# Kernel optimization log

Hardware: AMD Instinct MI355X
Metric: run time of the kernel (lower is better)

## Reference

```python
import jax, jax.numpy as jnp
import numpy as np

C, H, K, G = 256, 8, 32, 8
HD = C // H
SCALE = HD ** -0.5
POS_BND = int(0.8 * K * 1 ** 0.5)  # 25
RPE_NUM = 2 * POS_BND + 1          # 51
NW = 4096


def setup_inputs() -> dict:
    key = jax.random.key(0)
    ks = jax.random.split(key, 8)
    data = jax.random.normal(ks[0], (NW * (K + G), C), dtype=jnp.float32)
    # relative xyz offsets between points in a window; exercise the clamp
    rel_pos = jax.random.randint(ks[1], (NW, K, K, 3), -POS_BND - 5, POS_BND + 6).astype(jnp.int32)
    # additive mask: 0 for valid pairs, -100 for masked (padded) pairs
    keep = jax.random.bernoulli(ks[2], 0.9, (NW, K + G, K + G))
    mask = jnp.where(keep, 0.0, -100.0).astype(jnp.float32)
    qkv_w = jax.random.normal(ks[3], (C, 3 * C), dtype=jnp.float32) * (C ** -0.5)
    qkv_b = jnp.zeros((3 * C,), dtype=jnp.float32)
    proj_w = jax.random.normal(ks[4], (C, C), dtype=jnp.float32) * (C ** -0.5)
    proj_b = jnp.zeros((C,), dtype=jnp.float32)
    rpe_table = jax.random.normal(ks[5], (3 * RPE_NUM, H), dtype=jnp.float32) * 0.02
    return {"data": data, "rel_pos": rel_pos, "mask": mask, "qkv_w": qkv_w,
            "qkv_b": qkv_b, "proj_w": proj_w, "proj_b": proj_b, "rpe_table": rpe_table}


def reference(data, rel_pos, mask, qkv_w, qkv_b, proj_w, proj_b, rpe_table):
    W = K + G  # window size including context tokens
    qkv = data @ qkv_w + qkv_b                              # (T, 3C)
    qkv_std = jnp.std(qkv, axis=0, ddof=1)                  # torch .std is unbiased
    qkv = qkv.reshape(-1, W, 3, H, HD).transpose(2, 0, 3, 1, 4)  # (3, Nw, H, W, HD)
    q, k, v = qkv[0] * SCALE, qkv[1], qkv[2]
    attn = jnp.einsum('nhqd,nhkd->nhqk', q, k)              # (Nw, H, W, W)
    # RPE: clamp offsets, index per-axis slices of table, sum over xyz
    idx = jnp.clip(rel_pos, -POS_BND, POS_BND) + POS_BND + jnp.arange(3, dtype=rel_pos.dtype) * RPE_NUM
    rpe = rpe_table[idx].sum(axis=3)                        # (Nw, K, K, H)
    rpe = rpe.transpose(0, 3, 1, 2)                         # (Nw, H, K, K)
    rpe = jnp.pad(rpe, ((0, 0), (0, 0), (G, 0), (G, 0)))    # pad for context tokens
    attn = attn + rpe + mask[:, None]
    attn = jax.nn.softmax(attn, axis=-1)
    out = jnp.einsum('nhqk,nhkd->nqhd', attn, v).reshape(-1, W, C)
    out = out @ proj_w + proj_b                             # (Nw, W, C)
    return (out, qkv_std)
```

## Files before the change

### kernel.cpp

```cpp
#include <hip/hip_runtime.h>
#include <math.h>

#define SCALE_F 0.17677669529663687f

typedef __bf16 bf16x8 __attribute__((ext_vector_type(8)));
typedef float f32x4 __attribute__((ext_vector_type(4)));

__device__ __forceinline__ unsigned short f2bf(float f) {
  unsigned u = __builtin_bit_cast(unsigned, f);
  u = (u + 0x7FFFu + ((u >> 16) & 1u)) >> 16;
  return (unsigned short)u;
}
__device__ __forceinline__ float bf2f(unsigned short u) {
  return __builtin_bit_cast(float, (unsigned)u << 16);
}
__device__ __forceinline__ unsigned pk2(float a, float b) {
  return (unsigned)f2bf(a) | ((unsigned)f2bf(b) << 16);
}
__device__ __forceinline__ bf16x8 ld16(const void* p) {
  int4 v = *(const int4*)p;
  return __builtin_bit_cast(bf16x8, v);
}
__device__ __forceinline__ void gll16(const void* g, void* l) {
  __builtin_amdgcn_global_load_lds(
      (const __attribute__((address_space(1))) unsigned int*)g,
      (__attribute__((address_space(3))) unsigned int*)l, 16, 0, 0);
}


__global__ void octa_prep2(const float* __restrict__ qkv_w, const float* __restrict__ proj_w,
                           unsigned short* __restrict__ wTq, unsigned short* __restrict__ pTq)
{
  int e = blockIdx.x * 256 + threadIdx.x;
  if (e < 196608) {
    int nh = e / 98304, rr = e % 98304;
    int kc = rr / 12288, p2 = rr % 12288;
    int n = p2 >> 5, cw = p2 & 31;
    int kl = cw ^ (((n >> 1) & 3) << 3);
    wTq[e] = f2bf(qkv_w[(size_t)(kc * 32 + kl) * 768 + nh * 384 + n]);
  } else {
    int e2 = e - 196608;
    int kc = e2 >> 13, p2 = e2 & 8191;
    int n = p2 >> 5, cw = p2 & 31;
    int kl = cw ^ (((n >> 1) & 3) << 3);
    pTq[e2] = f2bf(proj_w[(size_t)(kc * 32 + kl) * 256 + n]);
  }
}

#define K1_A0 0
#define K1_A1 4096
#define K1_B0 8192
#define K1_B1 32768
#define K1_LDS 57344

__global__ __launch_bounds__(512, 4)
void octa_qkv(const float* __restrict__ data, const float* __restrict__ qkv_b,
              const unsigned short* __restrict__ wTq, float* __restrict__ ws,
              char* __restrict__ qg, char* __restrict__ kg, char* __restrict__ vg)
{
  extern __shared__ char smem[];
  const int tid = threadIdx.x, lane = tid & 63, wid = tid >> 6;
  const int ql = lane & 15, lg = lane >> 4;
  const int bm = blockIdx.x >> 1, nh = blockIdx.x & 1;
  const int wr = wid >> 2, wc = wid & 3;

  const int arow = tid >> 3, acq = tid & 7;
  const float* abase = data + ((size_t)bm * 64 + arow) * 256 + acq * 4;
  const int alds = arow * 64 + ((acq * 8) ^ (((arow >> 1) & 3) << 4));
  const char* wbase = (const char*)wTq + (size_t)nh * 196608;

  float4 arr0 = *(const float4*)(abase);
  float4 arr1 = *(const float4*)(abase + 32);
  #pragma unroll
  for (int it = 0; it < 3; ++it)
    gll16(wbase + wid * 3072 + it * 1024 + lane * 16,
          smem + K1_B0 + wid * 3072 + it * 1024);
  *(uint2*)(smem + K1_A0 + alds) = make_uint2(pk2(arr0.x, arr0.y), pk2(arr0.z, arr0.w));
  __syncthreads();

  f32x4 acc[2][6];
  #pragma unroll
  for (int m = 0; m < 2; ++m)
    #pragma unroll
    for (int n = 0; n < 6; ++n) acc[m][n] = (f32x4){0.f, 0.f, 0.f, 0.f};

  #pragma unroll
  for (int t = 0; t < 8; ++t) {
    if (t < 6) {
      float4 tmp = *(const float4*)(abase + (t + 2) * 32);
      if ((t & 1) == 0) arr0 = tmp; else arr1 = tmp;
    }
    if (t < 7) {
      char* bb1 = smem + (((t + 1) & 1) ? K1_B1 : K1_B0);
      #pragma unroll
      for (int it = 0; it < 3; ++it)
        gll16(wbase + (size_t)(t + 1) * 24576 + wid * 3072 + it * 1024 + lane * 16,
              bb1 + wid * 3072 + it * 1024);
    }
    const char* ab = smem + ((t & 1) ? K1_A1 : K1_A0);
    const char* bb = smem + ((t & 1) ? K1_B1 : K1_B0);
    bf16x8 af[2];
    #pragma unroll
    for (int mt = 0; mt < 2; ++mt) {
      int row = wr * 32 + mt * 16 + ql;
      af[mt] = ld16(ab + row * 64 + ((lg * 16) ^ (((row >> 1) & 3) << 4)));
    }
    #pragma unroll
    for (int nt = 0; nt < 6; ++nt) {
      int n = wc * 96 + nt * 16 + ql;
      bf16x8 bf = ld16(bb + n * 64 + ((lg * 16) ^ (((n >> 1) & 3) << 4)));
      #pragma unroll
      for (int mt = 0; mt < 2; ++mt)
        acc[mt][nt] = __builtin_amdgcn_mfma_f32_16x16x32_bf16(af[mt], bf, acc[mt][nt], 0, 0, 0);
    }
    if (t < 7) {
      float4 av = ((t + 1) & 1) ? arr1 : arr0;
      *(uint2*)(smem + ((t & 1) ? K1_A0 : K1_A1) + alds) =
          make_uint2(pk2(av.x, av.y), pk2(av.z, av.w));
    }
    __syncthreads();
  }

  #pragma unroll
  for (int nt = 0; nt < 6; ++nt) {
    int colg = nh * 384 + wc * 96 + nt * 16 + ql;
    int tensor = colg >> 8, h = (colg >> 5) & 7, d = colg & 31;
    float bias = qkv_b[colg];
    float s1 = 0.f, s2 = 0.f;
    #pragma unroll
    for (int mt = 0; mt < 2; ++mt) {
      float v4[4];
      #pragma unroll
      for (int r = 0; r < 4; ++r) {
        float v = acc[mt][nt][r] + bias;
        s1 += v; s2 += v * v;
        v4[r] = v;
      }
      int tg0 = bm * 64 + wr * 32 + mt * 16 + lg * 4;
      int w = tg0 / 40, tk0 = tg0 - w * 40;
      size_t slice = (size_t)(w * 8 + h) * 2560;
      if (tensor == 0) {
        #pragma unroll
        for (int r = 0; r < 4; ++r)
          *(unsigned short*)(qg + slice + (tk0 + r) * 64 + d * 2) = f2bf(v4[r] * SCALE_F);
      } else if (tensor == 1) {
        #pragma unroll
        for (int r = 0; r < 4; ++r)
          *(unsigned short*)(kg + slice + (tk0 + r) * 64 + d * 2) = f2bf(v4[r]);
      } else {
        *(uint2*)(vg + slice + d * 80 + tk0 * 2) =
            make_uint2(pk2(v4[0], v4[1]), pk2(v4[2], v4[3]));
      }
    }
    s1 += __shfl_xor(s1, 16); s1 += __shfl_xor(s1, 32);
    s2 += __shfl_xor(s2, 16); s2 += __shfl_xor(s2, 32);
    if (lg == 0) { atomicAdd(ws + colg, s1); atomicAdd(ws + 768 + colg, s2); }
  }
}

#define A2_MSK 0
#define A2_IDX 4160
#define A2_RPT 8256
#define A2_P   13376
#define A2_LDS 44096

__global__ __launch_bounds__(512, 4)
void octa_attn(const char* __restrict__ qg, const char* __restrict__ kg,
               const char* __restrict__ vg, const float* __restrict__ maskp,
               const int* __restrict__ rel_pos, const float* __restrict__ rpe_table,
               char* __restrict__ Og)
{
  extern __shared__ char smem[];
  const int tid = threadIdx.x, w = blockIdx.x, wid = tid >> 6;
  const int lane = tid & 63, ql = lane & 15, lg = lane >> 4, h = wid;
  const int perm = ql * 64 + lg * 16;
  const int vperm = ql * 80 + lg * 16;
  const char* qb = qg + (size_t)(w * 8 + h) * 2560;
  const char* kb = kg + (size_t)(w * 8 + h) * 2560;
  const char* vb = vg + (size_t)(w * 8 + h) * 2560;

  bf16x8 kf0 = ld16(kb + perm), kf1 = ld16(kb + 1024 + perm), kf2 = ld16(kb + 2048 + perm);
  bf16x8 qf0 = ld16(qb + perm), qf1 = ld16(qb + 1024 + perm), qf2 = ld16(qb + 2048 + perm);
  bf16x8 vA = ld16(vb + vperm);
  bf16x8 vB = ld16(vb + 1280 + vperm);
  bf16x8 vC = ld16(vb + 64 + vperm);
  bf16x8 vD = ld16(vb + 1280 + 64 + vperm);
  if (lg != 0) {
    int4 z = {0, 0, 0, 0};
    vC = __builtin_bit_cast(bf16x8, z);
    vD = __builtin_bit_cast(bf16x8, z);
  }

  for (int f = tid; f < 1600; f += 512) {
    float m = maskp[(size_t)w * 1600 + f];
    int qi = f / 40, kj = f - qi * 40;
    *(unsigned short*)(smem + A2_MSK + kj * 104 + qi * 2) = f2bf(m);
  }
  for (int f = tid; f < 1024; f += 512) {
    const int* rp = rel_pos + ((size_t)w * 1024 + f) * 3;
    int c0 = rp[0], c1 = rp[1], c2 = rp[2];
    c0 = min(25, max(-25, c0)); c1 = min(25, max(-25, c1)); c2 = min(25, max(-25, c2));
    unsigned pk = (unsigned)(c0 + 25) | ((unsigned)(c1 + 76) << 10) | ((unsigned)(c2 + 127) << 20);
    int qi8 = f >> 5, kj8 = f & 31;
    *(unsigned*)(smem + A2_IDX + kj8 * 128 + ((qi8 * 4) ^ ((kj8 & 1) << 6))) = pk;
  }
  for (int f = tid; f < 1224; f += 512)
    *(float*)(smem + A2_RPT + (((f & 7) * 160 + (f >> 3)) << 2)) = rpe_table[f];
  __syncthreads();

  f32x4 st[9];
  {
    bf16x8 kf[3] = {kf0, kf1, kf2}, qf[3] = {qf0, qf1, qf2};
    #pragma unroll
    for (int a = 0; a < 3; ++a)
      #pragma unroll
      for (int b = 0; b < 3; ++b)
        st[a * 3 + b] = __builtin_amdgcn_mfma_f32_16x16x32_bf16(
            kf[a], qf[b], (f32x4){0.f, 0.f, 0.f, 0.f}, 0, 0, 0);
  }

  float mx[3] = {-3e38f, -3e38f, -3e38f};
  #pragma unroll
  for (int a = 0; a < 3; ++a) {
    #pragma unroll
    for (int b = 0; b < 3; ++b) {
      #pragma unroll
      for (int r = 0; r < 4; ++r) {
        int kj = a * 16 + lg * 4 + r;
        int qi = b * 16 + ql;
        float s = st[a * 3 + b][r];
        if (kj < 40) {
          if (qi < 40) {
            s += bf2f(*(const unsigned short*)(smem + A2_MSK + kj * 104 + qi * 2));
            if (kj >= 8 && qi >= 8) {
              unsigned pk = *(const unsigned*)(smem + A2_IDX + (kj - 8) * 128 +
                                               (((qi - 8) * 4) ^ (((kj - 8) & 1) << 6)));
              s += *(const float*)(smem + A2_RPT + ((h * 160 + (pk & 1023)) << 2))
                 + *(const float*)(smem + A2_RPT + ((h * 160 + ((pk >> 10) & 1023)) << 2))
                 + *(const float*)(smem + A2_RPT + ((h * 160 + (pk >> 20)) << 2));
            }
          }
        } else {
          s = -1e30f;
        }
        st[a * 3 + b][r] = s;
        mx[b] = fmaxf(mx[b], s);
      }
    }
  }
  #pragma unroll
  for (int b = 0; b < 3; ++b) {
    mx[b] = fmaxf(mx[b], __shfl_xor(mx[b], 16));
    mx[b] = fmaxf(mx[b], __shfl_xor(mx[b], 32));
  }
  float sum[3] = {0.f, 0.f, 0.f};
  #pragma unroll
  for (int a = 0; a < 3; ++a)
    #pragma unroll
    for (int b = 0; b < 3; ++b)
      #pragma unroll
      for (int r = 0; r < 4; ++r) {
        float e = __expf(st[a * 3 + b][r] - mx[b]);
        st[a * 3 + b][r] = e;
        sum[b] += e;
      }
  float inv[3];
  #pragma unroll
  for (int b = 0; b < 3; ++b) {
    sum[b] += __shfl_xor(sum[b], 16);
    sum[b] += __shfl_xor(sum[b], 32);
    inv[b] = 1.f / sum[b];
  }

  char* pb_ = smem + A2_P + wid * 3840;
  f32x4 ot[6];
  #pragma unroll
  for (int i = 0; i < 6; ++i) ot[i] = (f32x4){0.f, 0.f, 0.f, 0.f};

  #pragma unroll
  for (int a = 0; a < 2; ++a)
    #pragma unroll
    for (int b = 0; b < 3; ++b)
      #pragma unroll
      for (int r = 0; r < 4; ++r) {
        int kj = a * 16 + lg * 4 + r, qi = b * 16 + ql;
        *(unsigned short*)(pb_ + qi * 80 + kj * 2) = f2bf(st[a * 3 + b][r] * inv[b]);
      }
  asm volatile("" ::: "memory");
  #pragma unroll
  for (int b = 0; b < 3; ++b) {
    bf16x8 pf = ld16(pb_ + (b * 16 + ql) * 80 + lg * 16);
    ot[b]     = __builtin_amdgcn_mfma_f32_16x16x32_bf16(vA, pf, ot[b], 0, 0, 0);
    ot[3 + b] = __builtin_amdgcn_mfma_f32_16x16x32_bf16(vB, pf, ot[3 + b], 0, 0, 0);
  }
  asm volatile("" ::: "memory");
  #pragma unroll
  for (int b = 0; b < 3; ++b) {
    int qi = b * 16 + ql;
    #pragma unroll
    for (int r = 0; r < 4; ++r)
      *(unsigned short*)(pb_ + qi * 80 + (lg * 4 + r) * 2) = f2bf(st[6 + b][r] * inv[b]);
    *(uint2*)(pb_ + qi * 80 + 32 + lg * 8) = make_uint2(0u, 0u);
  }
  asm volatile("" ::: "memory");
  #pragma unroll
  for (int b = 0; b < 3; ++b) {
    bf16x8 pf = ld16(pb_ + (b * 16 + ql) * 80 + lg * 16);
    ot[b]     = __builtin_amdgcn_mfma_f32_16x16x32_bf16(vC, pf, ot[b], 0, 0, 0);
    ot[3 + b] = __builtin_amdgcn_mfma_f32_16x16x32_bf16(vD, pf, ot[3 + b], 0, 0, 0);
  }

  __syncthreads();
  #pragma unroll
  for (int dm = 0; dm < 2; ++dm)
    #pragma unroll
    for (int b = 0; b < 3; ++b) {
      int qi = b * 16 + ql;
      if (b == 2 && ql >= 8) continue;
      unsigned u0 = pk2(ot[dm * 3 + b][0], ot[dm * 3 + b][1]);
      unsigned u1 = pk2(ot[dm * 3 + b][2], ot[dm * 3 + b][3]);
      int tg = w * 40 + qi;
      int colb = (h * 32 + dm * 16 + lg * 4) * 2;
      *(uint2*)(Og + (size_t)tg * 512 + (colb ^ (((tg >> 1) & 3) << 4))) = make_uint2(u0, u1);
    }
}

#define P3_A0 0
#define P3_A1 8192
#define P3_B0 16384
#define P3_B1 32768
#define P3_LDS 49152

__global__ __launch_bounds__(512, 4)
void octa_proj(const char* __restrict__ Og, const unsigned short* __restrict__ pTq,
               const float* __restrict__ proj_b, float* __restrict__ out)
{
  extern __shared__ char smem[];
  const int tid = threadIdx.x, lane = tid & 63, wid = tid >> 6;
  const int ql = lane & 15, lg = lane >> 4;
  const int bm = blockIdx.x;
  const int wr = wid >> 2, wc = wid & 3;
  const char* pbase = (const char*)pTq;

  gll16(Og + ((size_t)bm * 128 + (tid >> 2)) * 512 + (tid & 3) * 16,
        smem + P3_A0 + wid * 1024);
  #pragma unroll
  for (int it = 0; it < 2; ++it)
    gll16(pbase + (wid * 128 + it * 64 + lane) * 16, smem + P3_B0 + wid * 2048 + it * 1024);
  __syncthreads();

  f32x4 acc[4][4];
  #pragma unroll
  for (int m = 0; m < 4; ++m)
    #pragma unroll
    for (int n = 0; n < 4; ++n) acc[m][n] = (f32x4){0.f, 0.f, 0.f, 0.f};

  #pragma unroll
  for (int t = 0; t < 8; ++t) {
    if (t < 7) {
      char* ab1 = smem + (((t + 1) & 1) ? P3_A1 : P3_A0);
      char* bb1 = smem + (((t + 1) & 1) ? P3_B1 : P3_B0);
      gll16(Og + ((size_t)bm * 128 + (tid >> 2)) * 512 + (t + 1) * 64 + (tid & 3) * 16,
            ab1 + wid * 1024);
      #pragma unroll
      for (int it = 0; it < 2; ++it)
        gll16(pbase + (size_t)(t + 1) * 16384 + (wid * 128 + it * 64 + lane) * 16,
              bb1 + wid * 2048 + it * 1024);
    }
    const char* ab = smem + ((t & 1) ? P3_A1 : P3_A0);
    const char* bb = smem + ((t & 1) ? P3_B1 : P3_B0);
    bf16x8 af[4];
    #pragma unroll
    for (int mt = 0; mt < 4; ++mt) {
      int row = wr * 64 + mt * 16 + ql;
      af[mt] = ld16(ab + row * 64 + ((lg * 16) ^ (((row >> 1) & 3) << 4)));
    }
    #pragma unroll
    for (int nt = 0; nt < 4; ++nt) {
      int n = wc * 64 + nt * 16 + ql;
      bf16x8 bf = ld16(bb + n * 64 + ((lg * 16) ^ (((n >> 1) & 3) << 4)));
      #pragma unroll
      for (int mt = 0; mt < 4; ++mt)
        acc[mt][nt] = __builtin_amdgcn_mfma_f32_16x16x32_bf16(af[mt], bf, acc[mt][nt], 0, 0, 0);
    }
    __syncthreads();
  }

  #pragma unroll
  for (int nt = 0; nt < 4; ++nt) {
    int col = wc * 64 + nt * 16 + ql;
    float pb = proj_b[col];
    #pragma unroll
    for (int mt = 0; mt < 4; ++mt)
      #pragma unroll
      for (int r = 0; r < 4; ++r) {
        int tg = bm * 128 + wr * 64 + mt * 16 + lg * 4 + r;
        out[(size_t)tg * 256 + col] = acc[mt][nt][r] + pb;
      }
  }
}

__global__ void octa_std(const float* __restrict__ ws, float* __restrict__ out,
                         int total_rows, size_t off)
{
  int j = blockIdx.x * 256 + threadIdx.x;
  if (j < 768) {
    float s = ws[j], ss = ws[768 + j];
    float T = (float)total_rows;
    float var = (ss - s * s / T) / (T - 1.f);
    out[off + j] = sqrtf(fmaxf(var, 0.f));
  }
}

#define O_RPE 0
#define O_MSK 4896
#define O_IDX 8096
#define O_A   12192
#define O_ATT 36768
#define B1_SZ 49152
#define ATT_STRIDE 11776
#define AK 3840
#define AV 7680
#define B2_S (O_ATT + 94208)
#define B2_A O_ATT
#define LDS_BYTES_V4 163744

__device__ __forceinline__ int a_addr(int row, int byte) {
  return O_A + row * 512 + (byte ^ ((row & 7) << 4));
}
__device__ __forceinline__ int v_addr(int d, int byte) {
  return AV + d * 128 + (byte ^ ((d & 7) << 4));
}

__global__ void octa_prep_v4(const float* __restrict__ qkv_w, const float* __restrict__ proj_w,
                             unsigned short* __restrict__ wTq, unsigned short* __restrict__ pTq)
{
  int idx = blockIdx.x * 256 + threadIdx.x;
  if (idx < 196608) {
    int n = idx >> 8, k = idx & 255;
    wTq[idx] = f2bf(qkv_w[k * 768 + n]);
  } else {
    int i = idx - 196608;
    int n = i >> 8, k = i & 255;
    pTq[i] = f2bf(proj_w[k * 256 + n]);
  }
}

__global__ __launch_bounds__(512, 2)
void octa_main_v4(const float* __restrict__ data, const int* __restrict__ rel_pos,
                  const float* __restrict__ maskp, const float* __restrict__ qkv_b,
                  const float* __restrict__ proj_b, const float* __restrict__ rpe_table,
                  const unsigned short* __restrict__ wTq, const unsigned short* __restrict__ pTq,
                  float* __restrict__ ws, float* __restrict__ out)
{
  extern __shared__ char smem[];
  float* s_rpe = (float*)(smem + O_RPE);
  const int tid = threadIdx.x;
  const int w   = blockIdx.x;
  const int wid = tid >> 6;
  const int lane = tid & 63;
  const int ql = lane & 15;
  const int lg = lane >> 4;
  const int h  = wid;
  const int ab = O_ATT + wid * ATT_STRIDE;

  {
    #pragma unroll
    for (int it = 0; it < 6; ++it) {
      int g = it * 512 + tid;
      int n = g >> 2, slot = g & 3;
      const char* src = (const char*)wTq + (size_t)n * 512 + ((slot * 16) ^ ((n & 3) << 4));
      gll16(src, smem + O_ATT + it * 8192 + wid * 1024);
    }
  }
  for (int f = tid; f < 1224; f += 512) s_rpe[f] = rpe_table[f];
  for (int f = tid; f < 400; f += 512) {
    float4 m4 = ((const float4*)(maskp + (size_t)w * 1600))[f];
    uint2 pk;
    pk.x = pk2(m4.x, m4.y); pk.y = pk2(m4.z, m4.w);
    *(uint2*)(smem + O_MSK + f * 8) = pk;
  }
  for (int p = tid; p < 1024; p += 512) {
    const int* rp = rel_pos + ((size_t)w * 1024 + p) * 3;
    int c0 = rp[0], c1 = rp[1], c2 = rp[2];
    c0 = min(25, max(-25, c0)); c1 = min(25, max(-25, c1)); c2 = min(25, max(-25, c2));
    unsigned pk = (unsigned)(c0 + 25) | ((unsigned)(c1 + 76) << 10) | ((unsigned)(c2 + 127) << 20);
    *(unsigned*)(smem + O_IDX + ((p * 4) ^ (((p >> 5) & 7) << 4))) = pk;
  }
  {
    const float4* src = (const float4*)(data + (size_t)w * 10240);
    for (int f = tid; f < 2560; f += 512) {
      int token = f >> 6, q4 = f & 63;
      float4 d4 = src[f];
      uint2 pk;
      pk.x = pk2(d4.x, d4.y); pk.y = pk2(d4.z, d4.w);
      *(uint2*)(smem + a_addr(token, q4 * 8)) = pk;
    }
    int token = 40 + (tid >> 6), byte = (tid & 63) * 8;
    *(uint2*)(smem + a_addr(token, byte)) = make_uint2(0u, 0u);
  }
  __syncthreads();

  f32x4 acc[18];
  #pragma unroll
  for (int i = 0; i < 18; ++i) acc[i] = (f32x4){0.f, 0.f, 0.f, 0.f};

  for (int t = 0; t < 8; ++t) {
    if (t < 7) {
      int bb = O_ATT + ((t + 1) & 1) * B1_SZ;
      #pragma unroll
      for (int it = 0; it < 6; ++it) {
        int g = it * 512 + tid;
        int n = g >> 2, slot = g & 3;
        const char* src = (const char*)wTq + (size_t)n * 512 + (t + 1) * 64
                          + ((slot * 16) ^ ((n & 3) << 4));
        gll16(src, smem + bb + it * 8192 + wid * 1024);
      }
    }
    const int bb = O_ATT + (t & 1) * B1_SZ;
    bf16x8 af[3];
    #pragma unroll
    for (int mt = 0; mt < 3; ++mt)
      af[mt] = ld16(smem + a_addr(mt * 16 + ql, t * 64 + lg * 16));
    #pragma unroll
    for (int j = 0; j < 6; ++j) {
      int n = ((j >> 1) * 16 + 2 * wid + (j & 1)) * 16 + ql;
      bf16x8 bf = ld16(smem + bb + n * 64 + ((lg * 16) ^ ((n & 3) << 4)));
      #pragma unroll
      for (int mt = 0; mt < 3; ++mt)
        acc[j * 3 + mt] = __builtin_amdgcn_mfma_f32_16x16x32_bf16(af[mt], bf, acc[j * 3 + mt], 0, 0, 0);
    }
    __syncthreads();
  }

  {
    #pragma unroll
    for (int it = 0; it < 4; ++it) {
      int g = it * 512 + tid;
      int n = g >> 3, slot = g & 7;
      const char* src = (const char*)pTq + (size_t)n * 512 + ((slot * 16) ^ ((n & 7) << 4));
      gll16(src, smem + B2_S + it * 8192 + wid * 1024);
    }
  }

  #pragma unroll
  for (int j = 0; j < 6; ++j) {
    int sec = j >> 1;
    int ncol = sec * 256 + 32 * wid + (j & 1) * 16 + ql;
    int d = (j & 1) * 16 + ql;
    float bias = qkv_b[ncol];
    float s1 = 0.f, s2 = 0.f;
    #pragma unroll
    for (int mt = 0; mt < 3; ++mt) {
      #pragma unroll
      for (int r = 0; r < 4; ++r) {
        int token = mt * 16 + lg * 4 + r;
        float v = acc[j * 3 + mt][r] + bias;
        if (token < 40) { s1 += v; s2 += v * v; }
        if (sec == 0)
          *(unsigned short*)(smem + ab + token * 80 + d * 2) = f2bf(v * SCALE_F);
        else if (sec == 1)
          *(unsigned short*)(smem + ab + AK + token * 80 + d * 2) = f2bf(v);
        else
          *(unsigned short*)(smem + ab + v_addr(d, token * 2)) = f2bf(v);
      }
    }
    s1 += __shfl_xor(s1, 16); s1 += __shfl_xor(s1, 32);
    s2 += __shfl_xor(s2, 16); s2 += __shfl_xor(s2, 32);
    if (lg == 0) { atomicAdd(ws + ncol, s1); atomicAdd(ws + 768 + ncol, s2); }
  }
  {
    int zd = lane >> 1;
    int zb = 96 + (lane & 1) * 16;
    *(int4*)(smem + ab + v_addr(zd, zb)) = (int4){0, 0, 0, 0};
  }
  asm volatile("" ::: "memory");

  f32x4 st[9];
  {
    bf16x8 kf[3], qf[3];
    #pragma unroll
    for (int a = 0; a < 3; ++a) kf[a] = ld16(smem + ab + AK + (a * 16 + ql) * 80 + lg * 16);
    #pragma unroll
    for (int b = 0; b < 3; ++b) qf[b] = ld16(smem + ab + (b * 16 + ql) * 80 + lg * 16);
    #pragma unroll
    for (int a = 0; a < 3; ++a)
      #pragma unroll
      for (int b = 0; b < 3; ++b)
        st[a * 3 + b] = __builtin_amdgcn_mfma_f32_16x16x32_bf16(
            kf[a], qf[b], (f32x4){0.f, 0.f, 0.f, 0.f}, 0, 0, 0);
  }

  float mx[3] = {-3e38f, -3e38f, -3e38f};
  #pragma unroll
  for (int a = 0; a < 3; ++a) {
    #pragma unroll
    for (int b = 0; b < 3; ++b) {
      #pragma unroll
      for (int r = 0; r < 4; ++r) {
        int kj = a * 16 + lg * 4 + r;
        int qi = b * 16 + ql;
        float s = st[a * 3 + b][r];
        if (kj < 40) {
          if (qi < 40) {
            s += bf2f(*(const unsigned short*)(smem + O_MSK + (qi * 40 + kj) * 2));
            if (kj >= 8 && qi >= 8) {
              int p = (qi - 8) * 32 + (kj - 8);
              unsigned pk = *(const unsigned*)(smem + O_IDX + ((p * 4) ^ (((p >> 5) & 7) << 4)));
              s += s_rpe[(pk & 1023) * 8 + h] + s_rpe[((pk >> 10) & 1023) * 8 + h]
                 + s_rpe[(pk >> 20) * 8 + h];
            }
          }
        } else {
          s = -1e30f;
        }
        st[a * 3 + b][r] = s;
        mx[b] = fmaxf(mx[b], s);
      }
    }
  }
  #pragma unroll
  for (int b = 0; b < 3; ++b) {
    mx[b] = fmaxf(mx[b], __shfl_xor(mx[b], 16));
    mx[b] = fmaxf(mx[b], __shfl_xor(mx[b], 32));
  }
  float sum[3] = {0.f, 0.f, 0.f};
  #pragma unroll
  for (int a = 0; a < 3; ++a)
    #pragma unroll
    for (int b = 0; b < 3; ++b)
      #pragma unroll
      for (int r = 0; r < 4; ++r) {
        float e = __expf(st[a * 3 + b][r] - mx[b]);
        st[a * 3 + b][r] = e;
        sum[b] += e;
      }
  float inv[3];
  #pragma unroll
  for (int b = 0; b < 3; ++b) {
    sum[b] += __shfl_xor(sum[b], 16);
    sum[b] += __shfl_xor(sum[b], 32);
    inv[b] = 1.f / sum[b];
  }

  f32x4 ot[6];
  #pragma unroll
  for (int i = 0; i < 6; ++i) ot[i] = (f32x4){0.f, 0.f, 0.f, 0.f};

  #pragma unroll
  for (int a = 0; a < 2; ++a)
    #pragma unroll
    for (int b = 0; b < 3; ++b)
      #pragma unroll
      for (int r = 0; r < 4; ++r) {
        int kj = a * 16 + lg * 4 + r, qi = b * 16 + ql;
        *(unsigned short*)(smem + ab + qi * 80 + kj * 2) = f2bf(st[a * 3 + b][r] * inv[b]);
      }
  asm volatile("" ::: "memory");
  {
    bf16x8 vf0 = ld16(smem + ab + v_addr(ql, lg * 16));
    bf16x8 vf1 = ld16(smem + ab + v_addr(16 + ql, lg * 16));
    #pragma unroll
    for (int b = 0; b < 3; ++b) {
      bf16x8 pf = ld16(smem + ab + (b * 16 + ql) * 80 + lg * 16);
      ot[b] = __builtin_amdgcn_mfma_f32_16x16x32_bf16(vf0, pf, ot[b], 0, 0, 0);
      ot[3 + b] = __builtin_amdgcn_mfma_f32_16x16x32_bf16(vf1, pf, ot[3 + b], 0, 0, 0);
    }
  }
  asm volatile("" ::: "memory");
  #pragma unroll
  for (int b = 0; b < 3; ++b) {
    int qi = b * 16 + ql;
    #pragma unroll
    for (int r = 0; r < 4; ++r) {
      int kj = 32 + lg * 4 + r;
      *(unsigned short*)(smem + ab + qi * 80 + (kj - 32) * 2) = f2bf(st[6 + b][r] * inv[b]);
    }
    *(uint2*)(smem + ab + qi * 80 + 32 + lg * 8) = make_uint2(0u, 0u);
  }
  asm volatile("" ::: "memory");
  {
    bf16x8 vf0 = ld16(smem + ab + v_addr(ql, 64 + lg * 16));
    bf16x8 vf1 = ld16(smem + ab + v_addr(16 + ql, 64 + lg * 16));
    #pragma unroll
    for (int b = 0; b < 3; ++b) {
      bf16x8 pf = ld16(smem + ab + (b * 16 + ql) * 80 + lg * 16);
      ot[b] = __builtin_amdgcn_mfma_f32_16x16x32_bf16(vf0, pf, ot[b], 0, 0, 0);
      ot[3 + b] = __builtin_amdgcn_mfma_f32_16x16x32_bf16(vf1, pf, ot[3 + b], 0, 0, 0);
    }
  }
  #pragma unroll
  for (int dm = 0; dm < 2; ++dm)
    #pragma unroll
    for (int b = 0; b < 3; ++b)
      #pragma unroll
      for (int r = 0; r < 4; ++r) {
        int d = dm * 16 + lg * 4 + r;
        int qi = b * 16 + ql;
        *(unsigned short*)(smem + a_addr(qi, (h * 32 + d) * 2)) = f2bf(ot[dm * 3 + b][r]);
      }
  __syncthreads();

  f32x4 oacc[6];
  #pragma unroll
  for (int i = 0; i < 6; ++i) oacc[i] = (f32x4){0.f, 0.f, 0.f, 0.f};

  for (int t = 0; t < 4; ++t) {
    if (t < 3) {
      int bb = ((t + 1) & 1) ? B2_A : B2_S;
      #pragma unroll
      for (int it = 0; it < 4; ++it) {
        int g = it * 512 + tid;
        int n = g >> 3, slot = g & 7;
        const char* src = (const char*)pTq + (size_t)n * 512 + (t + 1) * 128
                          + ((slot * 16) ^ ((n & 7) << 4));
        gll16(src, smem + bb + it * 8192 + wid * 1024);
      }
    }
    const int bb = (t & 1) ? B2_A : B2_S;
    #pragma unroll
    for (int ks = 0; ks < 2; ++ks) {
      bf16x8 af[3];
      #pragma unroll
      for (int mt = 0; mt < 3; ++mt)
        af[mt] = ld16(smem + a_addr(mt * 16 + ql, t * 128 + ks * 64 + lg * 16));
      #pragma unroll
      for (int nt = 0; nt < 2; ++nt) {
        int n = (2 * wid + nt) * 16 + ql;
        bf16x8 bf = ld16(smem + bb + n * 128 + ((ks * 64 + lg * 16) ^ ((n & 7) << 4)));
        #pragma unroll
        for (int mt = 0; mt < 3; ++mt)
          oacc[nt * 3 + mt] = __builtin_amdgcn_mfma_f32_16x16x32_bf16(af[mt], bf, oacc[nt * 3 + mt], 0, 0, 0);
      }
    }
    __syncthreads();
  }

  #pragma unroll
  for (int nt = 0; nt < 2; ++nt) {
    int ncol = (2 * wid + nt) * 16 + ql;
    float pb = proj_b[ncol];
    #pragma unroll
    for (int mt = 0; mt < 3; ++mt)
      #pragma unroll
      for (int r = 0; r < 4; ++r) {
        int token = mt * 16 + lg * 4 + r;
        if (token < 40)
          out[(size_t)w * 10240 + token * 256 + ncol] = oacc[nt * 3 + mt][r] + pb;
      }
  }
}

extern "C" void kernel_launch(void* const* d_in, const int* in_sizes, int n_in,
                              void* d_out, int out_size, void* d_ws, size_t ws_size,
                              hipStream_t stream) {
  const float* data    = (const float*)d_in[0];
  const int*   rel_pos = (const int*)d_in[1];
  const float* maskp   = (const float*)d_in[2];
  const float* qkv_w   = (const float*)d_in[3];
  const float* qkv_b   = (const float*)d_in[4];
  const float* proj_w  = (const float*)d_in[5];
  const float* proj_b  = (const float*)d_in[6];
  const float* rpe_tab = (const float*)d_in[7];
  float* out = (float*)d_out;
  float* ws  = (float*)d_ws;

  const int nw = in_sizes[1] / 3072;
  const int total_rows = nw * 40;
  const size_t std_off = (size_t)nw * 10240;

  const size_t WS_NEED = 530432ull + 83886080ull;

  unsigned short* wTq = (unsigned short*)((char*)d_ws + 6144);
  unsigned short* pTq = (unsigned short*)((char*)d_ws + 399360);

  hipMemsetAsync(ws, 0, 6144, stream);

  if (ws_size >= WS_NEED) {
    char* kg = (char*)d_ws + 530432;
    char* Og = kg;
    char* qg = (char*)d_out;
    char* vg = (char*)d_out + 83886080;

    hipLaunchKernelGGL(octa_prep2, dim3(1024), dim3(256), 0, stream, qkv_w, proj_w, wTq, pTq);
    hipLaunchKernelGGL(octa_qkv, dim3(nw * 40 / 64 * 2), dim3(512), K1_LDS, stream,
                       data, qkv_b, wTq, ws, qg, kg, vg);
    hipLaunchKernelGGL(octa_attn, dim3(nw), dim3(512), A2_LDS, stream,
                       qg, kg, vg, maskp, rel_pos, rpe_tab, Og);
    hipLaunchKernelGGL(octa_proj, dim3(nw * 40 / 128), dim3(512), P3_LDS, stream,
                       Og, pTq, proj_b, out);
    hipLaunchKernelGGL(octa_std, dim3(3), dim3(256), 0, stream, ws, out, total_rows, std_off);
  } else {
    hipLaunchKernelGGL(octa_prep_v4, dim3(1024), dim3(256), 0, stream, qkv_w, proj_w, wTq, pTq);
    (void)hipFuncSetAttribute((const void*)octa_main_v4,
                              hipFuncAttributeMaxDynamicSharedMemorySize, LDS_BYTES_V4);
    hipLaunchKernelGGL(octa_main_v4, dim3(nw), dim3(512), LDS_BYTES_V4, stream,
                       data, rel_pos, maskp, qkv_b, proj_b, rpe_tab, wTq, pTq, ws, out);
    hipLaunchKernelGGL(octa_std, dim3(3), dim3(256), 0, stream, ws, out, total_rows, std_off);
  }
}
```

Measured before the change: 416.2 us.

## Load QKV A-operand straight into MFMA registers, bypassing LDS staging

The QKV GEMM kernel no longer stages the fp32 input tile through LDS. Each wave now loads its own rows directly from global memory in the MFMA fragment layout, double-buffered in registers, and converts them to bf16 on the fly. Only the weight tile remains in LDS, which shrinks the allocation and can allow more resident blocks. Synchronisation uses manual vmcnt waits, raw barriers and sched_barriers. The trade-off is that waves sharing the same rows now issue redundant global loads of the input, and correctness depends on the hand-counted vmcnt bookkeeping.

```diff
diff --git a/kernel.cpp b/kernel.cpp
--- a/kernel.cpp
+++ b/kernel.cpp
@@ -19,6 +19,12 @@
 }
 __device__ __forceinline__ bf16x8 ld16(const void* p) {
   int4 v = *(const int4*)p;
+  return __builtin_bit_cast(bf16x8, v);
+}
+__device__ __forceinline__ bf16x8 cvt8(float4 x, float4 y) {
+  int4 v;
+  v.x = (int)pk2(x.x, x.y); v.y = (int)pk2(x.z, x.w);
+  v.z = (int)pk2(y.x, y.y); v.w = (int)pk2(y.z, y.w);
   return __builtin_bit_cast(bf16x8, v);
 }
 __device__ __forceinline__ void gll16(const void* g, void* l) {
@@ -47,11 +53,9 @@
   }
 }
 
-#define K1_A0 0
-#define K1_A1 4096
-#define K1_B0 8192
-#define K1_B1 32768
-#define K1_LDS 57344
+#define K2_B0 0
+#define K2_B1 24576
+#define K2_LDS 49152
 
 __global__ __launch_bounds__(512, 4)
 void octa_qkv(const float* __restrict__ data, const float* __restrict__ qkv_b,
@@ -64,19 +68,26 @@
   const int bm = blockIdx.x >> 1, nh = blockIdx.x & 1;
   const int wr = wid >> 2, wc = wid & 3;
 
-  const int arow = tid >> 3, acq = tid & 7;
-  const float* abase = data + ((size_t)bm * 64 + arow) * 256 + acq * 4;
-  const int alds = arow * 64 + ((acq * 8) ^ (((arow >> 1) & 3) << 4));
+  const float* a0 = data + ((size_t)bm * 64 + wr * 32 + ql) * 256 + lg * 8;
+  const float* a1 = a0 + 16 * 256;
   const char* wbase = (const char*)wTq + (size_t)nh * 196608;
 
-  float4 arr0 = *(const float4*)(abase);
-  float4 arr1 = *(const float4*)(abase + 32);
   #pragma unroll
   for (int it = 0; it < 3; ++it)
     gll16(wbase + wid * 3072 + it * 1024 + lane * 16,
-          smem + K1_B0 + wid * 3072 + it * 1024);
-  *(uint2*)(smem + K1_A0 + alds) = make_uint2(pk2(arr0.x, arr0.y), pk2(arr0.z, arr0.w));
-  __syncthreads();
+          smem + K2_B0 + wid * 3072 + it * 1024);
+  __builtin_amdgcn_sched_barrier(0);
+  float4 Ab[2][4];
+  Ab[0][0] = *(const float4*)(a0);
+  Ab[0][1] = *(const float4*)(a0 + 4);
+  Ab[0][2] = *(const float4*)(a1);
+  Ab[0][3] = *(const float4*)(a1 + 4);
+  __builtin_amdgcn_sched_barrier(0);
+  Ab[1][0] = *(const float4*)(a0 + 32);
+  Ab[1][1] = *(const float4*)(a0 + 36);
+  Ab[1][2] = *(const float4*)(a1 + 32);
+  Ab[1][3] = *(const float4*)(a1 + 36);
+  __builtin_amdgcn_sched_barrier(0);
 
   f32x4 acc[2][6];
   #pragma unroll
@@ -86,39 +97,38 @@
 
   #pragma unroll
   for (int t = 0; t < 8; ++t) {
-    if (t < 6) {
-      float4 tmp = *(const float4*)(abase + (t + 2) * 32);
-      if ((t & 1) == 0) arr0 = tmp; else arr1 = tmp;
-    }
+    if (t < 7) asm volatile("s_waitcnt vmcnt(4)" ::: "memory");
+    else       asm volatile("s_waitcnt vmcnt(0)" ::: "memory");
+    __builtin_amdgcn_s_barrier();
+    __builtin_amdgcn_sched_barrier(0);
+
+    bf16x8 af0 = cvt8(Ab[t & 1][0], Ab[t & 1][1]);
+    bf16x8 af1 = cvt8(Ab[t & 1][2], Ab[t & 1][3]);
+    const char* bb = smem + ((t & 1) ? K2_B1 : K2_B0);
+    #pragma unroll
+    for (int nt = 0; nt < 6; ++nt) {
+      int n = wc * 96 + nt * 16 + ql;
+      bf16x8 bf = ld16(bb + n * 64 + ((lg * 16) ^ (((n >> 1) & 3) << 4)));
+      acc[0][nt] = __builtin_amdgcn_mfma_f32_16x16x32_bf16(af0, bf, acc[0][nt], 0, 0, 0);
+      acc[1][nt] = __builtin_amdgcn_mfma_f32_16x16x32_bf16(af1, bf, acc[1][nt], 0, 0, 0);
+    }
+    __builtin_amdgcn_sched_barrier(0);
+
     if (t < 7) {
-      char* bb1 = smem + (((t + 1) & 1) ? K1_B1 : K1_B0);
+      char* bb1 = smem + (((t + 1) & 1) ? K2_B1 : K2_B0);
       #pragma unroll
       for (int it = 0; it < 3; ++it)
         gll16(wbase + (size_t)(t + 1) * 24576 + wid * 3072 + it * 1024 + lane * 16,
               bb1 + wid * 3072 + it * 1024);
     }
-    const char* ab = smem + ((t & 1) ? K1_A1 : K1_A0);
-    const char* bb = smem + ((t & 1) ? K1_B1 : K1_B0);
-    bf16x8 af[2];
-    #pragma unroll
-    for (int mt = 0; mt < 2; ++mt) {
-      int row = wr * 32 + mt * 16 + ql;
-      af[mt] = ld16(ab + row * 64 + ((lg * 16) ^ (((row >> 1) & 3) << 4)));
-    }
-    #pragma unroll
-    for (int nt = 0; nt < 6; ++nt) {
-      int n = wc * 96 + nt * 16 + ql;
-      bf16x8 bf = ld16(bb + n * 64 + ((lg * 16) ^ (((n >> 1) & 3) << 4)));
-      #pragma unroll
-      for (int mt = 0; mt < 2; ++mt)
-        acc[mt][nt] = __builtin_amdgcn_mfma_f32_16x16x32_bf16(af[mt], bf, acc[mt][nt], 0, 0, 0);
-    }
-    if (t < 7) {
-      float4 av = ((t + 1) & 1) ? arr1 : arr0;
-      *(uint2*)(smem + ((t & 1) ? K1_A0 : K1_A1) + alds) =
-          make_uint2(pk2(av.x, av.y), pk2(av.z, av.w));
-    }
-    __syncthreads();
+    __builtin_amdgcn_sched_barrier(0);
+    if (t < 6) {
+      Ab[t & 1][0] = *(const float4*)(a0 + (t + 2) * 32);
+      Ab[t & 1][1] = *(const float4*)(a0 + (t + 2) * 32 + 4);
+      Ab[t & 1][2] = *(const float4*)(a1 + (t + 2) * 32);
+      Ab[t & 1][3] = *(const float4*)(a1 + (t + 2) * 32 + 4);
+    }
+    __builtin_amdgcn_sched_barrier(0);
   }
 
   #pragma unroll
@@ -783,7 +793,7 @@
     char* vg = (char*)d_out + 83886080;
 
     hipLaunchKernelGGL(octa_prep2, dim3(1024), dim3(256), 0, stream, qkv_w, proj_w, wTq, pTq);
-    hipLaunchKernelGGL(octa_qkv, dim3(nw * 40 / 64 * 2), dim3(512), K1_LDS, stream,
+    hipLaunchKernelGGL(octa_qkv, dim3(nw * 40 / 64 * 2), dim3(512), K2_LDS, stream,
                        data, qkv_b, wTq, ws, qg, kg, vg);
     hipLaunchKernelGGL(octa_attn, dim3(nw), dim3(512), A2_LDS, stream,
                        qg, kg, vg, maskp, rel_pos, rpe_tab, Og);
```

New measurement: 490.4 us. +17.8%, slower.

## Restructure QKV GEMM to stream weights from global and stage only activations

Applied to the files above, without the earlier changes.

The QKV projection kernel now processes 32-row activation tiles with all 768 output columns per block. It converts the full 32x256 activation tile into swizzled LDS once, and each wave reads its weight fragments straight from global memory (L2) in a plain transposed [n][k] layout. This removes the per-k-step LDS double buffering, global_load_lds weight staging and barriers, and cuts LDS use so more blocks can be resident. The cost is that every block re-reads the whole bf16 weight matrix from cache without LDS reuse, and the weight loads are no longer overlapped with compute by software pipelining.

```diff
diff --git a/kernel.cpp b/kernel.cpp
--- a/kernel.cpp
+++ b/kernel.cpp
@@ -33,11 +33,8 @@
 {
   int e = blockIdx.x * 256 + threadIdx.x;
   if (e < 196608) {
-    int nh = e / 98304, rr = e % 98304;
-    int kc = rr / 12288, p2 = rr % 12288;
-    int n = p2 >> 5, cw = p2 & 31;
-    int kl = cw ^ (((n >> 1) & 3) << 3);
-    wTq[e] = f2bf(qkv_w[(size_t)(kc * 32 + kl) * 768 + nh * 384 + n]);
+    int n = e >> 8, k = e & 255;
+    wTq[e] = f2bf(qkv_w[(size_t)k * 768 + n]);
   } else {
     int e2 = e - 196608;
     int kc = e2 >> 13, p2 = e2 & 8191;
@@ -47,11 +44,7 @@
   }
 }
 
-#define K1_A0 0
-#define K1_A1 4096
-#define K1_B0 8192
-#define K1_B1 32768
-#define K1_LDS 57344
+#define KQ_LDS 16384
 
 __global__ __launch_bounds__(512, 4)
 void octa_qkv(const float* __restrict__ data, const float* __restrict__ qkv_b,
@@ -61,23 +54,23 @@
   extern __shared__ char smem[];
   const int tid = threadIdx.x, lane = tid & 63, wid = tid >> 6;
   const int ql = lane & 15, lg = lane >> 4;
-  const int bm = blockIdx.x >> 1, nh = blockIdx.x & 1;
-  const int wr = wid >> 2, wc = wid & 3;
-
-  const int arow = tid >> 3, acq = tid & 7;
-  const float* abase = data + ((size_t)bm * 64 + arow) * 256 + acq * 4;
-  const int alds = arow * 64 + ((acq * 8) ^ (((arow >> 1) & 3) << 4));
-  const char* wbase = (const char*)wTq + (size_t)nh * 196608;
-
-  float4 arr0 = *(const float4*)(abase);
-  float4 arr1 = *(const float4*)(abase + 32);
-  #pragma unroll
-  for (int it = 0; it < 3; ++it)
-    gll16(wbase + wid * 3072 + it * 1024 + lane * 16,
-          smem + K1_B0 + wid * 3072 + it * 1024);
-  *(uint2*)(smem + K1_A0 + alds) = make_uint2(pk2(arr0.x, arr0.y), pk2(arr0.z, arr0.w));
+  const int bm = blockIdx.x;
+
+  {
+    const float4* src = (const float4*)(data + (size_t)bm * 32 * 256);
+    #pragma unroll
+    for (int rep = 0; rep < 4; ++rep) {
+      int f = rep * 512 + tid;
+      int row = f >> 6, q4 = f & 63;
+      float4 d4 = src[f];
+      *(uint2*)(smem + row * 512 + ((q4 * 8) ^ ((row & 7) << 4))) =
+          make_uint2(pk2(d4.x, d4.y), pk2(d4.z, d4.w));
+    }
+  }
   __syncthreads();
 
+  const char* wb = (const char*)wTq + (size_t)(wid * 96 + ql) * 512 + lg * 16;
+
   f32x4 acc[2][6];
   #pragma unroll
   for (int m = 0; m < 2; ++m)
@@ -86,44 +79,26 @@
 
   #pragma unroll
   for (int t = 0; t < 8; ++t) {
-    if (t < 6) {
-      float4 tmp = *(const float4*)(abase + (t + 2) * 32);
-      if ((t & 1) == 0) arr0 = tmp; else arr1 = tmp;
-    }
-    if (t < 7) {
-      char* bb1 = smem + (((t + 1) & 1) ? K1_B1 : K1_B0);
-      #pragma unroll
-      for (int it = 0; it < 3; ++it)
-        gll16(wbase + (size_t)(t + 1) * 24576 + wid * 3072 + it * 1024 + lane * 16,
-              bb1 + wid * 3072 + it * 1024);
-    }
-    const char* ab = smem + ((t & 1) ? K1_A1 : K1_A0);
-    const char* bb = smem + ((t & 1) ? K1_B1 : K1_B0);
+    bf16x8 bfr[6];
+    #pragma unroll
+    for (int nt = 0; nt < 6; ++nt)
+      bfr[nt] = ld16(wb + nt * 8192 + t * 64);
     bf16x8 af[2];
     #pragma unroll
     for (int mt = 0; mt < 2; ++mt) {
-      int row = wr * 32 + mt * 16 + ql;
-      af[mt] = ld16(ab + row * 64 + ((lg * 16) ^ (((row >> 1) & 3) << 4)));
+      int row = mt * 16 + ql;
+      af[mt] = ld16(smem + row * 512 + ((t * 64 + lg * 16) ^ ((row & 7) << 4)));
     }
     #pragma unroll
     for (int nt = 0; nt < 6; ++nt) {
-      int n = wc * 96 + nt * 16 + ql;
-      bf16x8 bf = ld16(bb + n * 64 + ((lg * 16) ^ (((n >> 1) & 3) << 4)));
-      #pragma unroll
-      for (int mt = 0; mt < 2; ++mt)
-        acc[mt][nt] = __builtin_amdgcn_mfma_f32_16x16x32_bf16(af[mt], bf, acc[mt][nt], 0, 0, 0);
-    }
-    if (t < 7) {
-      float4 av = ((t + 1) & 1) ? arr1 : arr0;
-      *(uint2*)(smem + ((t & 1) ? K1_A0 : K1_A1) + alds) =
-          make_uint2(pk2(av.x, av.y), pk2(av.z, av.w));
-    }
-    __syncthreads();
+      acc[0][nt] = __builtin_amdgcn_mfma_f32_16x16x32_bf16(af[0], bfr[nt], acc[0][nt], 0, 0, 0);
+      acc[1][nt] = __builtin_amdgcn_mfma_f32_16x16x32_bf16(af[1], bfr[nt], acc[1][nt], 0, 0, 0);
+    }
   }
 
   #pragma unroll
   for (int nt = 0; nt < 6; ++nt) {
-    int colg = nh * 384 + wc * 96 + nt * 16 + ql;
+    int colg = wid * 96 + nt * 16 + ql;
     int tensor = colg >> 8, h = (colg >> 5) & 7, d = colg & 31;
     float bias = qkv_b[colg];
     float s1 = 0.f, s2 = 0.f;
@@ -136,7 +111,7 @@
         s1 += v; s2 += v * v;
         v4[r] = v;
       }
-      int tg0 = bm * 64 + wr * 32 + mt * 16 + lg * 4;
+      int tg0 = bm * 32 + mt * 16 + lg * 4;
       int w = tg0 / 40, tk0 = tg0 - w * 40;
       size_t slice = (size_t)(w * 8 + h) * 2560;
       if (tensor == 0) {
@@ -783,7 +758,7 @@
     char* vg = (char*)d_out + 83886080;
 
     hipLaunchKernelGGL(octa_prep2, dim3(1024), dim3(256), 0, stream, qkv_w, proj_w, wTq, pTq);
-    hipLaunchKernelGGL(octa_qkv, dim3(nw * 40 / 64 * 2), dim3(512), K1_LDS, stream,
+    hipLaunchKernelGGL(octa_qkv, dim3(nw * 40 / 32), dim3(512), KQ_LDS, stream,
                        data, qkv_b, wTq, ws, qg, kg, vg);
     hipLaunchKernelGGL(octa_attn, dim3(nw), dim3(512), A2_LDS, stream,
                        qg, kg, vg, maskp, rel_pos, rpe_tab, Og);
```

Measured after the change: 505.3 us. +21.4%, slower.

## Stage QKV epilogue through LDS for coalesced stores and preload full A tile

Applied to the files above, without the earlier changes.

The QKV projection kernel now loads the whole 64x256 activation tile into LDS up front instead of double-buffering it per k-step. The epilogue first writes bf16 results into a swizzled LDS staging buffer, then emits 16-byte coalesced global stores in place of scattered 2-byte stores. V is now stored token-major like Q and K, so the attention kernel gathers V fragments with per-element 2-byte loads to build the transposed operand. LDS use per block rises to 80 KB, which may cut occupancy, and the attention kernel's V loads become much less efficient.

```diff
diff --git a/kernel.cpp b/kernel.cpp
--- a/kernel.cpp
+++ b/kernel.cpp
@@ -47,11 +47,11 @@
   }
 }
 
-#define K1_A0 0
-#define K1_A1 4096
-#define K1_B0 8192
-#define K1_B1 32768
-#define K1_LDS 57344
+#define KQ_A  0
+#define KQ_B0 32768
+#define KQ_B1 57344
+#define KQ_E  32768
+#define KQ_LDS 81920
 
 __global__ __launch_bounds__(512, 4)
 void octa_qkv(const float* __restrict__ data, const float* __restrict__ qkv_b,
@@ -63,19 +63,23 @@
   const int ql = lane & 15, lg = lane >> 4;
   const int bm = blockIdx.x >> 1, nh = blockIdx.x & 1;
   const int wr = wid >> 2, wc = wid & 3;
-
-  const int arow = tid >> 3, acq = tid & 7;
-  const float* abase = data + ((size_t)bm * 64 + arow) * 256 + acq * 4;
-  const int alds = arow * 64 + ((acq * 8) ^ (((arow >> 1) & 3) << 4));
   const char* wbase = (const char*)wTq + (size_t)nh * 196608;
 
-  float4 arr0 = *(const float4*)(abase);
-  float4 arr1 = *(const float4*)(abase + 32);
   #pragma unroll
   for (int it = 0; it < 3; ++it)
     gll16(wbase + wid * 3072 + it * 1024 + lane * 16,
-          smem + K1_B0 + wid * 3072 + it * 1024);
-  *(uint2*)(smem + K1_A0 + alds) = make_uint2(pk2(arr0.x, arr0.y), pk2(arr0.z, arr0.w));
+          smem + KQ_B0 + wid * 3072 + it * 1024);
+  {
+    const float4* src = (const float4*)(data + (size_t)bm * 64 * 256);
+    #pragma unroll
+    for (int rep = 0; rep < 8; ++rep) {
+      int f = rep * 512 + tid;
+      int row = f >> 6, q4 = f & 63;
+      float4 d4 = src[f];
+      *(uint2*)(smem + KQ_A + row * 512 + ((q4 * 8) ^ ((row & 7) << 4))) =
+          make_uint2(pk2(d4.x, d4.y), pk2(d4.z, d4.w));
+    }
+  }
   __syncthreads();
 
   f32x4 acc[2][6];
@@ -86,75 +90,64 @@
 
   #pragma unroll
   for (int t = 0; t < 8; ++t) {
-    if (t < 6) {
-      float4 tmp = *(const float4*)(abase + (t + 2) * 32);
-      if ((t & 1) == 0) arr0 = tmp; else arr1 = tmp;
-    }
     if (t < 7) {
-      char* bb1 = smem + (((t + 1) & 1) ? K1_B1 : K1_B0);
+      char* bb1 = smem + (((t + 1) & 1) ? KQ_B1 : KQ_B0);
       #pragma unroll
       for (int it = 0; it < 3; ++it)
         gll16(wbase + (size_t)(t + 1) * 24576 + wid * 3072 + it * 1024 + lane * 16,
               bb1 + wid * 3072 + it * 1024);
     }
-    const char* ab = smem + ((t & 1) ? K1_A1 : K1_A0);
-    const char* bb = smem + ((t & 1) ? K1_B1 : K1_B0);
+    const char* bb = smem + ((t & 1) ? KQ_B1 : KQ_B0);
     bf16x8 af[2];
     #pragma unroll
     for (int mt = 0; mt < 2; ++mt) {
       int row = wr * 32 + mt * 16 + ql;
-      af[mt] = ld16(ab + row * 64 + ((lg * 16) ^ (((row >> 1) & 3) << 4)));
+      af[mt] = ld16(smem + KQ_A + row * 512 + ((t * 64 + lg * 16) ^ ((row & 7) << 4)));
     }
     #pragma unroll
     for (int nt = 0; nt < 6; ++nt) {
       int n = wc * 96 + nt * 16 + ql;
       bf16x8 bf = ld16(bb + n * 64 + ((lg * 16) ^ (((n >> 1) & 3) << 4)));
-      #pragma unroll
-      for (int mt = 0; mt < 2; ++mt)
-        acc[mt][nt] = __builtin_amdgcn_mfma_f32_16x16x32_bf16(af[mt], bf, acc[mt][nt], 0, 0, 0);
-    }
-    if (t < 7) {
-      float4 av = ((t + 1) & 1) ? arr1 : arr0;
-      *(uint2*)(smem + ((t & 1) ? K1_A0 : K1_A1) + alds) =
-          make_uint2(pk2(av.x, av.y), pk2(av.z, av.w));
+      acc[0][nt] = __builtin_amdgcn_mfma_f32_16x16x32_bf16(af[0], bf, acc[0][nt], 0, 0, 0);
+      acc[1][nt] = __builtin_amdgcn_mfma_f32_16x16x32_bf16(af[1], bf, acc[1][nt], 0, 0, 0);
     }
     __syncthreads();
   }
 
   #pragma unroll
   for (int nt = 0; nt < 6; ++nt) {
-    int colg = nh * 384 + wc * 96 + nt * 16 + ql;
-    int tensor = colg >> 8, h = (colg >> 5) & 7, d = colg & 31;
-    float bias = qkv_b[colg];
+    int col_l = wc * 96 + nt * 16 + ql;
+    int gcol = nh * 384 + col_l;
+    int tensor = gcol >> 8;
+    float bias = qkv_b[gcol];
     float s1 = 0.f, s2 = 0.f;
     #pragma unroll
-    for (int mt = 0; mt < 2; ++mt) {
-      float v4[4];
-      #pragma unroll
-      for (int r = 0; r < 4; ++r) {
+    for (int mt = 0; mt < 2; ++mt)
+      #pragma unroll
+      for (int r = 0; r < 4; ++r) {
+        int tok = wr * 32 + mt * 16 + lg * 4 + r;
         float v = acc[mt][nt][r] + bias;
         s1 += v; s2 += v * v;
-        v4[r] = v;
-      }
-      int tg0 = bm * 64 + wr * 32 + mt * 16 + lg * 4;
-      int w = tg0 / 40, tk0 = tg0 - w * 40;
-      size_t slice = (size_t)(w * 8 + h) * 2560;
-      if (tensor == 0) {
-        #pragma unroll
-        for (int r = 0; r < 4; ++r)
-          *(unsigned short*)(qg + slice + (tk0 + r) * 64 + d * 2) = f2bf(v4[r] * SCALE_F);
-      } else if (tensor == 1) {
-        #pragma unroll
-        for (int r = 0; r < 4; ++r)
-          *(unsigned short*)(kg + slice + (tk0 + r) * 64 + d * 2) = f2bf(v4[r]);
-      } else {
-        *(uint2*)(vg + slice + d * 80 + tk0 * 2) =
-            make_uint2(pk2(v4[0], v4[1]), pk2(v4[2], v4[3]));
-      }
-    }
+        float sv = (tensor == 0) ? v * SCALE_F : v;
+        *(unsigned short*)(smem + KQ_E + tok * 768 + ((col_l * 2) ^ ((tok & 7) << 4))) = f2bf(sv);
+      }
     s1 += __shfl_xor(s1, 16); s1 += __shfl_xor(s1, 32);
     s2 += __shfl_xor(s2, 16); s2 += __shfl_xor(s2, 32);
-    if (lg == 0) { atomicAdd(ws + colg, s1); atomicAdd(ws + 768 + colg, s2); }
+    if (lg == 0) { atomicAdd(ws + gcol, s1); atomicAdd(ws + 768 + gcol, s2); }
+  }
+  __syncthreads();
+
+  #pragma unroll
+  for (int rep = 0; rep < 6; ++rep) {
+    int c = rep * 512 + tid;
+    int tok_l = c / 48, cc = c - tok_l * 48;
+    int4 val = *(const int4*)(smem + KQ_E + tok_l * 768 + ((cc * 16) ^ ((tok_l & 7) << 4)));
+    int gcol0 = nh * 384 + cc * 8;
+    int tensor = gcol0 >> 8, h = (gcol0 >> 5) & 7, d0 = gcol0 & 31;
+    int tg = bm * 64 + tok_l, w = tg / 40, tk = tg - w * 40;
+    size_t slice = (size_t)(w * 8 + h) * 2560;
+    char* base = tensor == 0 ? qg : (tensor == 1 ? kg : vg);
+    *(int4*)(base + slice + tk * 64 + d0 * 2) = val;
   }
 }
 
@@ -174,22 +167,31 @@
   const int tid = threadIdx.x, w = blockIdx.x, wid = tid >> 6;
   const int lane = tid & 63, ql = lane & 15, lg = lane >> 4, h = wid;
   const int perm = ql * 64 + lg * 16;
-  const int vperm = ql * 80 + lg * 16;
   const char* qb = qg + (size_t)(w * 8 + h) * 2560;
   const char* kb = kg + (size_t)(w * 8 + h) * 2560;
   const char* vb = vg + (size_t)(w * 8 + h) * 2560;
 
   bf16x8 kf0 = ld16(kb + perm), kf1 = ld16(kb + 1024 + perm), kf2 = ld16(kb + 2048 + perm);
   bf16x8 qf0 = ld16(qb + perm), qf1 = ld16(qb + 1024 + perm), qf2 = ld16(qb + 2048 + perm);
-  bf16x8 vA = ld16(vb + vperm);
-  bf16x8 vB = ld16(vb + 1280 + vperm);
-  bf16x8 vC = ld16(vb + 64 + vperm);
-  bf16x8 vD = ld16(vb + 1280 + 64 + vperm);
-  if (lg != 0) {
-    int4 z = {0, 0, 0, 0};
-    vC = __builtin_bit_cast(bf16x8, z);
-    vD = __builtin_bit_cast(bf16x8, z);
-  }
+  union U8 { unsigned short u[8]; bf16x8 v; };
+  U8 ua, ub, uc, ud;
+  #pragma unroll
+  for (int j = 0; j < 8; ++j) {
+    int tok = lg * 8 + j;
+    ua.u[j] = *(const unsigned short*)(vb + tok * 64 + ql * 2);
+    ub.u[j] = *(const unsigned short*)(vb + tok * 64 + (16 + ql) * 2);
+  }
+  if (lg == 0) {
+    #pragma unroll
+    for (int j = 0; j < 8; ++j) {
+      uc.u[j] = *(const unsigned short*)(vb + (32 + j) * 64 + ql * 2);
+      ud.u[j] = *(const unsigned short*)(vb + (32 + j) * 64 + (16 + ql) * 2);
+    }
+  } else {
+    #pragma unroll
+    for (int j = 0; j < 8; ++j) { uc.u[j] = 0; ud.u[j] = 0; }
+  }
+  bf16x8 vA = ua.v, vB = ub.v, vC = uc.v, vD = ud.v;
 
   for (int f = tid; f < 1600; f += 512) {
     float m = maskp[(size_t)w * 1600 + f];
@@ -782,8 +784,11 @@
     char* qg = (char*)d_out;
     char* vg = (char*)d_out + 83886080;
 
+    (void)hipFuncSetAttribute((const void*)octa_qkv,
+                              hipFuncAttributeMaxDynamicSharedMemorySize, KQ_LDS);
+
     hipLaunchKernelGGL(octa_prep2, dim3(1024), dim3(256), 0, stream, qkv_w, proj_w, wTq, pTq);
-    hipLaunchKernelGGL(octa_qkv, dim3(nw * 40 / 64 * 2), dim3(512), K1_LDS, stream,
+    hipLaunchKernelGGL(octa_qkv, dim3(nw * 40 / 64 * 2), dim3(512), KQ_LDS, stream,
                        data, qkv_b, wTq, ws, qg, kg, vg);
     hipLaunchKernelGGL(octa_attn, dim3(nw), dim3(512), A2_LDS, stream,
                        qg, kg, vg, maskp, rel_pos, rpe_tab, Og);
```

Measured after the change: 399.1 us. 1.04x faster.
